# Performance work log

Measured on AMD Instinct MI355X. Metric: run time of the kernel, lower is better.

Reference implementation:

```python
import jax, jax.numpy as jnp
import numpy as np

NUM_GRAPHS = 64


def gcn_conv(x, W, b, src, dst, inv_sqrt_deg, n_nodes):
    # PyG GCNConv: h = D^{-1/2}(A+I)D^{-1/2} X W + b (self-loops already in src/dst)
    h = x @ W  # [N, D_out]
    norm = inv_sqrt_deg[src] * inv_sqrt_deg[dst]  # [E+N]
    msg = h[src] * norm[:, None]  # gather + scale
    agg = jax.ops.segment_sum(msg, dst, num_segments=n_nodes)  # scatter-add
    return agg + b


def setup_inputs() -> dict:
    key = jax.random.key(0)
    ks = jax.random.split(key, 12)
    N, E, D_in, D_h, D_out = 50000, 800000, 256, 256, 128

    def glorot(k, shape):
        lim = np.sqrt(6.0 / (shape[0] + shape[1]))
        return jax.random.uniform(k, shape, jnp.float32, -lim, lim)

    x = jax.random.normal(ks[0], (N, D_in), jnp.float32)
    edge_index = jax.random.randint(ks[1], (2, E), 0, N, jnp.int64)
    batch = jnp.sort(jax.random.randint(ks[2], (N,), 0, NUM_GRAPHS, jnp.int64))
    return {
        "x": x,
        "edge_index": edge_index,
        "batch": batch,
        "W0": glorot(ks[3], (D_in, D_h)), "b0": jnp.zeros((D_h,), jnp.float32),
        "W1": glorot(ks[4], (D_h, D_h)), "b1": jnp.zeros((D_h,), jnp.float32),
        "W2": glorot(ks[5], (D_h, D_h)), "b2": jnp.zeros((D_h,), jnp.float32),
        "fc1_w": glorot(ks[6], (D_h, D_h)), "fc1_b": jnp.zeros((D_h,), jnp.float32),
        "fc2_w": glorot(ks[7], (D_h, D_out)), "fc2_b": jnp.zeros((D_out,), jnp.float32),
    }


def reference(x, edge_index, batch, W0, b0, W1, b1, W2, b2, fc1_w, fc1_b, fc2_w, fc2_b):
    n_nodes = x.shape[0]
    loops = jnp.arange(n_nodes, dtype=edge_index.dtype)
    src = jnp.concatenate([edge_index[0], loops])  # add self-loops
    dst = jnp.concatenate([edge_index[1], loops])
    deg = jax.ops.segment_sum(jnp.ones_like(dst, dtype=x.dtype), dst, num_segments=n_nodes)
    inv_sqrt_deg = jnp.where(deg > 0, jax.lax.rsqrt(jnp.maximum(deg, 1.0)), 0.0)

    h = jax.nn.relu(gcn_conv(x, W0, b0, src, dst, inv_sqrt_deg, n_nodes))
    h = jax.nn.relu(gcn_conv(h, W1, b1, src, dst, inv_sqrt_deg, n_nodes))
    h = jax.nn.relu(gcn_conv(h, W2, b2, src, dst, inv_sqrt_deg, n_nodes))

    # global_mean_pool over batch segment ids
    sums = jax.ops.segment_sum(h, batch, num_segments=NUM_GRAPHS)
    counts = jax.ops.segment_sum(jnp.ones((n_nodes,), h.dtype), batch, num_segments=NUM_GRAPHS)
    pooled = sums / jnp.maximum(counts, 1.0)[:, None]  # [NUM_GRAPHS, D_h]

    out = jax.nn.relu(pooled @ fc1_w + fc1_b)
    out = out @ fc2_w + fc2_b  # [NUM_GRAPHS, D_out]
    return out
```

## Files before the change

kernel.cpp:

```cpp
#include <hip/hip_runtime.h>
#include <stdint.h>

#define D_FEAT 256
#define NGRAPH 64
#define NSPLIT 8
#define BM 64
#define BK 32
#define LDR 40
#define SCAN_CHUNK 1024

using f32x4 = __attribute__((ext_vector_type(4))) float;
using s16x8 = __attribute__((ext_vector_type(8))) short;
using s16x4 = __attribute__((ext_vector_type(4))) short;
using i32x4 = __attribute__((ext_vector_type(4))) int;

__device__ __forceinline__ unsigned short f2bf(float f) {
  union { float f; unsigned u; } v; v.f = f;
  return (unsigned short)((v.u + 0x7FFFu + ((v.u >> 16) & 1u)) >> 16);
}
__device__ __forceinline__ float bf2f(unsigned short h) {
  union { unsigned u; float f; } v; v.u = ((unsigned)h) << 16; return v.f;
}
__device__ __forceinline__ f32x4 bf4_to_f32(s16x4 v) {
  f32x4 r;
  r.x = bf2f((unsigned short)v.x);
  r.y = bf2f((unsigned short)v.y);
  r.z = bf2f((unsigned short)v.z);
  r.w = bf2f((unsigned short)v.w);
  return r;
}

__global__ void hist_k(const int* __restrict__ dst, int* __restrict__ counts, int E) {
  int e = blockIdx.x * blockDim.x + threadIdx.x;
  if (e < E) atomicAdd(&counts[dst[e]], 1);
}

__global__ __launch_bounds__(256) void bsum_k(const int* __restrict__ counts,
                                              int* __restrict__ bsum, int N) {
  int base = blockIdx.x * SCAN_CHUNK;
  int t = threadIdx.x;
  int idx = base + t * 4;
  int s = 0;
  if (idx + 3 < N) {
    i32x4 v = *(const i32x4*)(counts + idx);
    s = v.x + v.y + v.z + v.w;
  } else {
    for (int j = 0; j < 4; ++j) if (idx + j < N) s += counts[idx + j];
  }
  for (int d = 1; d < 64; d <<= 1) s += __shfl_xor(s, d);
  __shared__ int ws[4];
  if ((t & 63) == 0) ws[t >> 6] = s;
  __syncthreads();
  if (t == 0) bsum[blockIdx.x] = ws[0] + ws[1] + ws[2] + ws[3];
}

__global__ __launch_bounds__(1024) void bscan_k(const int* __restrict__ bsum,
                                                int* __restrict__ boff,
                                                int* __restrict__ offN, int nb) {
  __shared__ int part[1024];
  int t = threadIdx.x;
  int v = (t < nb) ? bsum[t] : 0;
  part[t] = v;
  __syncthreads();
  for (int d = 1; d < 1024; d <<= 1) {
    int u = (t >= d) ? part[t - d] : 0;
    __syncthreads();
    part[t] += u;
    __syncthreads();
  }
  if (t < nb) boff[t] = part[t] - v;
  if (t == 1023) offN[0] = part[1023];
}

__global__ __launch_bounds__(256) void fillscan_k(const int* __restrict__ counts,
                                                  const int* __restrict__ boff,
                                                  int* __restrict__ off, int* __restrict__ cur,
                                                  float* __restrict__ isd, int N) {
  int b = blockIdx.x;
  int base = b * SCAN_CHUNK;
  int t = threadIdx.x;
  int idx = base + t * 4;
  int c[4];
  int s = 0;
  for (int j = 0; j < 4; ++j) {
    c[j] = (idx + j < N) ? counts[idx + j] : 0;
    s += c[j];
  }
  int inc = s;
  int lane = t & 63;
  for (int d = 1; d < 64; d <<= 1) {
    int u = __shfl_up(inc, d);
    if (lane >= d) inc += u;
  }
  __shared__ int wtot[4];
  if (lane == 63) wtot[t >> 6] = inc;
  __syncthreads();
  int woff = 0;
  for (int w = 0; w < (t >> 6); ++w) woff += wtot[w];
  int ex = boff[b] + woff + inc - s;
  for (int j = 0; j < 4; ++j) {
    int i = idx + j;
    if (i < N) {
      off[i] = ex;
      cur[i] = ex;
      isd[i] = rsqrtf((float)(c[j] + 1));
      ex += c[j];
    }
  }
}

__global__ void fill_k(const int* __restrict__ src, const int* __restrict__ dst,
                       int* __restrict__ cur, int* __restrict__ csr, int E) {
  int e = blockIdx.x * blockDim.x + threadIdx.x;
  if (e < E) {
    int d = dst[e];
    int pos = atomicAdd(&cur[d], 1);
    csr[pos] = src[e];
  }
}

__global__ void wconv_k(const float* __restrict__ W0, const float* __restrict__ W1,
                        const float* __restrict__ W2, unsigned short* __restrict__ Wt) {
  int idx = blockIdx.x * blockDim.x + threadIdx.x;
  int w = idx >> 16; int r = idx & 65535;
  int k = r >> 8, n = r & 255;
  const float* W = (w == 0) ? W0 : (w == 1) ? W1 : W2;
  Wt[(size_t)w * 65536 + n * 256 + k] = f2bf(W[k * 256 + n]);
}

template <bool F32IN>
__global__ __launch_bounds__(256) void gemm_k(const void* __restrict__ Xv,
                                              const unsigned short* __restrict__ Wt,
                                              unsigned short* __restrict__ P,
                                              const float* __restrict__ isd, int M) {
  __shared__ __align__(16) short As[BM * LDR];
  __shared__ __align__(16) short Bs[D_FEAT * LDR];
  int t = threadIdx.x;
  int lane = t & 63;
  int wave = t >> 6;
  int row0 = blockIdx.x * BM;
  int l15 = lane & 15;
  int l4  = lane >> 4;

  f32x4 acc[4][4];
  for (int m = 0; m < 4; ++m)
    for (int n = 0; n < 4; ++n)
      acc[m][n] = (f32x4){0.f, 0.f, 0.f, 0.f};

  for (int k0 = 0; k0 < D_FEAT; k0 += BK) {
    if constexpr (F32IN) {
      const float* X = (const float*)Xv;
      for (int i = 0; i < 2; ++i) {
        int g = t + i * 256;
        int r = g >> 3, c4 = g & 7;
        int grow = row0 + r;
        f32x4 v = (f32x4){0.f, 0.f, 0.f, 0.f};
        if (grow < M) v = *(const f32x4*)(X + (size_t)grow * D_FEAT + k0 + c4 * 4);
        s16x4 b;
        b.x = (short)f2bf(v.x); b.y = (short)f2bf(v.y);
        b.z = (short)f2bf(v.z); b.w = (short)f2bf(v.w);
        *(s16x4*)&As[r * LDR + c4 * 4] = b;
      }
    } else {
      const unsigned short* X = (const unsigned short*)Xv;
      int r = t >> 2, c = t & 3;
      int grow = row0 + r;
      s16x8 v = {0, 0, 0, 0, 0, 0, 0, 0};
      if (grow < M) v = *(const s16x8*)(X + (size_t)grow * D_FEAT + k0 + c * 8);
      *(s16x8*)&As[r * LDR + c * 8] = v;
    }
    for (int i = 0; i < 4; ++i) {
      int g = t + i * 256;
      int n = g >> 2, c = g & 3;
      i32x4 v = *(const i32x4*)(Wt + (size_t)n * D_FEAT + k0 + c * 8);
      *(i32x4*)&Bs[n * LDR + c * 8] = v;
    }
    __syncthreads();
    s16x8 a[4], b[4];
    for (int m = 0; m < 4; ++m)
      a[m] = *(const s16x8*)&As[(m * 16 + l15) * LDR + l4 * 8];
    for (int n = 0; n < 4; ++n)
      b[n] = *(const s16x8*)&Bs[(wave * 64 + n * 16 + l15) * LDR + l4 * 8];
    for (int m = 0; m < 4; ++m)
      for (int n = 0; n < 4; ++n)
        acc[m][n] = __builtin_amdgcn_mfma_f32_16x16x32_bf16(a[m], b[n], acc[m][n], 0, 0, 0);
    __syncthreads();
  }

  for (int m = 0; m < 4; ++m) {
    int rbase = row0 + m * 16 + l4 * 4;
    for (int r = 0; r < 4; ++r) {
      int row = rbase + r;
      if (row >= M) continue;
      float sc = isd[row];
      for (int n = 0; n < 4; ++n) {
        int col = wave * 64 + n * 16 + l15;
        P[(size_t)row * D_FEAT + col] = f2bf(acc[m][n][r] * sc);
      }
    }
  }
}

__global__ __launch_bounds__(256) void agg_k(const unsigned short* __restrict__ P,
                                             const int* __restrict__ csr,
                                             const int* __restrict__ off,
                                             const float* __restrict__ isd,
                                             const float* __restrict__ bias,
                                             unsigned short* __restrict__ H, int N) {
  int gid = blockIdx.x * blockDim.x + threadIdx.x;
  int node = gid >> 6;
  int lane = gid & 63;
  if (node >= N) return;
  const s16x4* P4 = (const s16x4*)P;
  f32x4 acc = bf4_to_f32(P4[(size_t)node * 64 + lane]);
  int lo = off[node], hi = off[node + 1];
  int e = lo;
  for (; e + 3 < hi; e += 4) {
    int s0 = csr[e], s1 = csr[e + 1], s2 = csr[e + 2], s3 = csr[e + 3];
    s16x4 v0 = P4[(size_t)s0 * 64 + lane];
    s16x4 v1 = P4[(size_t)s1 * 64 + lane];
    s16x4 v2 = P4[(size_t)s2 * 64 + lane];
    s16x4 v3 = P4[(size_t)s3 * 64 + lane];
    acc += bf4_to_f32(v0);
    acc += bf4_to_f32(v1);
    acc += bf4_to_f32(v2);
    acc += bf4_to_f32(v3);
  }
  for (; e < hi; ++e) {
    acc += bf4_to_f32(P4[(size_t)csr[e] * 64 + lane]);
  }
  float sc = isd[node];
  f32x4 bb = *(const f32x4*)(bias + lane * 4);
  s16x4 o;
  o.x = (short)f2bf(fmaxf(acc.x * sc + bb.x, 0.f));
  o.y = (short)f2bf(fmaxf(acc.y * sc + bb.y, 0.f));
  o.z = (short)f2bf(fmaxf(acc.z * sc + bb.z, 0.f));
  o.w = (short)f2bf(fmaxf(acc.w * sc + bb.w, 0.f));
  ((s16x4*)H)[(size_t)node * 64 + lane] = o;
}

__device__ __forceinline__ int lower_bound_batch(const int* __restrict__ b, int N, int v) {
  int lo = 0, hi = N;
  while (lo < hi) { int mid = (lo + hi) >> 1; if (b[mid] < v) lo = mid + 1; else hi = mid; }
  return lo;
}

__global__ __launch_bounds__(256) void pool_k(const unsigned short* __restrict__ H,
                                              const int* __restrict__ batch,
                                              float* __restrict__ pp, int N) {
  int g = blockIdx.x >> 3;
  int s = blockIdx.x & (NSPLIT - 1);
  int c = threadIdx.x;
  int lo = lower_bound_batch(batch, N, g);
  int hi = lower_bound_batch(batch, N, g + 1);
  int len = hi - lo;
  int slo = lo + (int)(((long long)len * s) >> 3);
  int shi = lo + (int)(((long long)len * (s + 1)) >> 3);
  float sum = 0.f;
  for (int i = slo; i < shi; ++i) sum += bf2f(H[(size_t)i * D_FEAT + c]);
  pp[(g * NSPLIT + s) * D_FEAT + c] = sum;
}

__global__ __launch_bounds__(256) void fc_k(const float* __restrict__ pp,
                                            const int* __restrict__ batch,
                                            const float* __restrict__ fc1w, const float* __restrict__ fc1b,
                                            const float* __restrict__ fc2w, const float* __restrict__ fc2b,
                                            float* __restrict__ out, int N) {
  __shared__ float pl[D_FEAT];
  __shared__ float h1[D_FEAT];
  int g = blockIdx.x, j = threadIdx.x;
  int lo = lower_bound_batch(batch, N, g);
  int hi = lower_bound_batch(batch, N, g + 1);
  float cnt = fmaxf((float)(hi - lo), 1.f);
  float sum = 0.f;
  for (int s = 0; s < NSPLIT; ++s) sum += pp[(g * NSPLIT + s) * D_FEAT + j];
  pl[j] = sum / cnt;
  __syncthreads();
  float a = fc1b[j];
  for (int k = 0; k < D_FEAT; ++k) a += pl[k] * fc1w[k * D_FEAT + j];
  h1[j] = fmaxf(a, 0.f);
  __syncthreads();
  if (j < 128) {
    float o = fc2b[j];
    for (int k = 0; k < D_FEAT; ++k) o += h1[k] * fc2w[k * 128 + j];
    out[g * 128 + j] = o;
  }
}

extern "C" void kernel_launch(void* const* d_in, const int* in_sizes, int n_in,
                              void* d_out, int out_size, void* d_ws, size_t ws_size,
                              hipStream_t stream) {
  const float* x    = (const float*)d_in[0];
  const int*   ei   = (const int*)d_in[1];
  const int*   batch= (const int*)d_in[2];
  const float* W0   = (const float*)d_in[3];
  const float* b0   = (const float*)d_in[4];
  const float* W1   = (const float*)d_in[5];
  const float* b1   = (const float*)d_in[6];
  const float* W2   = (const float*)d_in[7];
  const float* b2   = (const float*)d_in[8];
  const float* fc1w = (const float*)d_in[9];
  const float* fc1b = (const float*)d_in[10];
  const float* fc2w = (const float*)d_in[11];
  const float* fc2b = (const float*)d_in[12];
  float* out = (float*)d_out;

  int N = in_sizes[0] / D_FEAT;
  int E = in_sizes[1] / 2;
  const int* srcE = ei;
  const int* dstE = ei + E;
  int nb = (N + SCAN_CHUNK - 1) / SCAN_CHUNK;

  char* w = (char*)d_ws;
  auto alloc = [&](size_t bytes) { char* p = w; w += (bytes + 255) & ~(size_t)255; return p; };
  int*   counts = (int*)  alloc((size_t)N * 4);
  int*   off    = (int*)  alloc((size_t)(N + 1) * 4);
  int*   cur    = (int*)  alloc((size_t)N * 4);
  float* isd    = (float*)alloc((size_t)N * 4);
  int*   csr    = (int*)  alloc((size_t)E * 4);
  int*   bsum   = (int*)  alloc((size_t)nb * 4);
  int*   boff   = (int*)  alloc((size_t)nb * 4);
  unsigned short* Wt = (unsigned short*)alloc((size_t)3 * 65536 * 2);
  unsigned short* P = (unsigned short*)alloc((size_t)N * D_FEAT * 2);
  unsigned short* H = (unsigned short*)alloc((size_t)N * D_FEAT * 2);
  float* pp     = (float*)alloc((size_t)NGRAPH * NSPLIT * D_FEAT * 4);

  hipMemsetAsync(counts, 0, (size_t)N * 4, stream);
  hist_k<<<(E + 255) / 256, 256, 0, stream>>>(dstE, counts, E);
  bsum_k<<<nb, 256, 0, stream>>>(counts, bsum, N);
  bscan_k<<<1, 1024, 0, stream>>>(bsum, boff, off + N, nb);
  fillscan_k<<<nb, 256, 0, stream>>>(counts, boff, off, cur, isd, N);
  fill_k<<<(E + 255) / 256, 256, 0, stream>>>(srcE, dstE, cur, csr, E);
  wconv_k<<<768, 256, 0, stream>>>(W0, W1, W2, Wt);

  int gblocks = (N + BM - 1) / BM;
  int ablocks = (N * 64 + 255) / 256;

  gemm_k<true> <<<gblocks, 256, 0, stream>>>(x, Wt,             P, isd, N);
  agg_k        <<<ablocks, 256, 0, stream>>>(P, csr, off, isd, b0, H, N);
  gemm_k<false><<<gblocks, 256, 0, stream>>>(H, Wt + 65536,     P, isd, N);
  agg_k        <<<ablocks, 256, 0, stream>>>(P, csr, off, isd, b1, H, N);
  gemm_k<false><<<gblocks, 256, 0, stream>>>(H, Wt + 2 * 65536, P, isd, N);
  agg_k        <<<ablocks, 256, 0, stream>>>(P, csr, off, isd, b2, H, N);

  pool_k<<<NGRAPH * NSPLIT, 256, 0, stream>>>(H, batch, pp, N);
  fc_k  <<<NGRAPH, 256, 0, stream>>>(pp, batch, fc1w, fc1b, fc2w, fc2b, out, N);
}
```

Before: 409.1 us.

## Pad CSR rows to even length and aggregate two neighbors per wave with 16B loads

Each node's CSR segment is padded to an even edge count, with padding entries pointing to an extra zero row appended to P and H. The aggregation kernel splits the wave into two halves. Each half gathers a different neighbor with 16-byte vector loads, and the halves are combined with a cross-lane shuffle. This aims to double memory-level parallelism and widen the gather loads. In exchange it adds an init kernel, padded storage, wasted gathers on the pad rows, and a reduction step where half the wave sits idle at write-out.

```diff
diff --git a/kernel.cpp b/kernel.cpp
--- a/kernel.cpp
+++ b/kernel.cpp
@@ -21,14 +21,6 @@
 __device__ __forceinline__ float bf2f(unsigned short h) {
   union { unsigned u; float f; } v; v.u = ((unsigned)h) << 16; return v.f;
 }
-__device__ __forceinline__ f32x4 bf4_to_f32(s16x4 v) {
-  f32x4 r;
-  r.x = bf2f((unsigned short)v.x);
-  r.y = bf2f((unsigned short)v.y);
-  r.z = bf2f((unsigned short)v.z);
-  r.w = bf2f((unsigned short)v.w);
-  return r;
-}
 
 __global__ void hist_k(const int* __restrict__ dst, int* __restrict__ counts, int E) {
   int e = blockIdx.x * blockDim.x + threadIdx.x;
@@ -41,11 +33,8 @@
   int t = threadIdx.x;
   int idx = base + t * 4;
   int s = 0;
-  if (idx + 3 < N) {
-    i32x4 v = *(const i32x4*)(counts + idx);
-    s = v.x + v.y + v.z + v.w;
-  } else {
-    for (int j = 0; j < 4; ++j) if (idx + j < N) s += counts[idx + j];
+  for (int j = 0; j < 4; ++j) {
+    if (idx + j < N) { int c = counts[idx + j]; s += c + (c & 1); }
   }
   for (int d = 1; d < 64; d <<= 1) s += __shfl_xor(s, d);
   __shared__ int ws[4];
@@ -80,11 +69,12 @@
   int base = b * SCAN_CHUNK;
   int t = threadIdx.x;
   int idx = base + t * 4;
-  int c[4];
+  int c[4], cp[4];
   int s = 0;
   for (int j = 0; j < 4; ++j) {
     c[j] = (idx + j < N) ? counts[idx + j] : 0;
-    s += c[j];
+    cp[j] = c[j] + (c[j] & 1);
+    s += cp[j];
   }
   int inc = s;
   int lane = t & 63;
@@ -104,8 +94,23 @@
       off[i] = ex;
       cur[i] = ex;
       isd[i] = rsqrtf((float)(c[j] + 1));
-      ex += c[j];
+      ex += cp[j];
     }
+  }
+}
+
+__global__ __launch_bounds__(256) void csrinit_k(int* __restrict__ csr, int cap4,
+                                                 unsigned int* __restrict__ Prow,
+                                                 unsigned int* __restrict__ Hrow, int N) {
+  int t = blockIdx.x * blockDim.x + threadIdx.x;
+  if (t < cap4) {
+    i32x4 v = (i32x4){N, N, N, N};
+    ((i32x4*)csr)[t] = v;
+  }
+  if (blockIdx.x == 0) {
+    int j = threadIdx.x;
+    if (j < 128) Prow[j] = 0u;
+    else Hrow[j - 128] = 0u;
   }
 }
 
@@ -209,34 +214,58 @@
                                              unsigned short* __restrict__ H, int N) {
   int gid = blockIdx.x * blockDim.x + threadIdx.x;
   int node = gid >> 6;
+  if (node >= N) return;
   int lane = gid & 63;
-  if (node >= N) return;
-  const s16x4* P4 = (const s16x4*)P;
-  f32x4 acc = bf4_to_f32(P4[(size_t)node * 64 + lane]);
+  int half = lane >> 5;
+  int col  = lane & 31;
+  const s16x8* P8 = (const s16x8*)P;
+
+  float acc[8];
+  {
+    int si = half ? N : node;
+    s16x8 v = P8[(size_t)si * 32 + col];
+    for (int j = 0; j < 8; ++j) acc[j] = bf2f((unsigned short)v[j]);
+  }
+
   int lo = off[node], hi = off[node + 1];
   int e = lo;
-  for (; e + 3 < hi; e += 4) {
-    int s0 = csr[e], s1 = csr[e + 1], s2 = csr[e + 2], s3 = csr[e + 3];
-    s16x4 v0 = P4[(size_t)s0 * 64 + lane];
-    s16x4 v1 = P4[(size_t)s1 * 64 + lane];
-    s16x4 v2 = P4[(size_t)s2 * 64 + lane];
-    s16x4 v3 = P4[(size_t)s3 * 64 + lane];
-    acc += bf4_to_f32(v0);
-    acc += bf4_to_f32(v1);
-    acc += bf4_to_f32(v2);
-    acc += bf4_to_f32(v3);
-  }
-  for (; e < hi; ++e) {
-    acc += bf4_to_f32(P4[(size_t)csr[e] * 64 + lane]);
-  }
-  float sc = isd[node];
-  f32x4 bb = *(const f32x4*)(bias + lane * 4);
-  s16x4 o;
-  o.x = (short)f2bf(fmaxf(acc.x * sc + bb.x, 0.f));
-  o.y = (short)f2bf(fmaxf(acc.y * sc + bb.y, 0.f));
-  o.z = (short)f2bf(fmaxf(acc.z * sc + bb.z, 0.f));
-  o.w = (short)f2bf(fmaxf(acc.w * sc + bb.w, 0.f));
-  ((s16x4*)H)[(size_t)node * 64 + lane] = o;
+  for (; e + 8 <= hi; e += 8) {
+    int i0 = csr[e + 0 + half];
+    int i1 = csr[e + 2 + half];
+    int i2 = csr[e + 4 + half];
+    int i3 = csr[e + 6 + half];
+    s16x8 v0 = P8[(size_t)i0 * 32 + col];
+    s16x8 v1 = P8[(size_t)i1 * 32 + col];
+    s16x8 v2 = P8[(size_t)i2 * 32 + col];
+    s16x8 v3 = P8[(size_t)i3 * 32 + col];
+    for (int j = 0; j < 8; ++j) acc[j] += bf2f((unsigned short)v0[j]);
+    for (int j = 0; j < 8; ++j) acc[j] += bf2f((unsigned short)v1[j]);
+    for (int j = 0; j < 8; ++j) acc[j] += bf2f((unsigned short)v2[j]);
+    for (int j = 0; j < 8; ++j) acc[j] += bf2f((unsigned short)v3[j]);
+  }
+  for (; e < hi; e += 2) {
+    int i = csr[e + half];
+    s16x8 v = P8[(size_t)i * 32 + col];
+    for (int j = 0; j < 8; ++j) acc[j] += bf2f((unsigned short)v[j]);
+  }
+
+  for (int j = 0; j < 8; ++j) acc[j] += __shfl_xor(acc[j], 32);
+
+  if (half == 0) {
+    float sc = isd[node];
+    f32x4 b0 = *(const f32x4*)(bias + col * 8);
+    f32x4 b1 = *(const f32x4*)(bias + col * 8 + 4);
+    s16x8 o;
+    o[0] = (short)f2bf(fmaxf(acc[0] * sc + b0.x, 0.f));
+    o[1] = (short)f2bf(fmaxf(acc[1] * sc + b0.y, 0.f));
+    o[2] = (short)f2bf(fmaxf(acc[2] * sc + b0.z, 0.f));
+    o[3] = (short)f2bf(fmaxf(acc[3] * sc + b0.w, 0.f));
+    o[4] = (short)f2bf(fmaxf(acc[4] * sc + b1.x, 0.f));
+    o[5] = (short)f2bf(fmaxf(acc[5] * sc + b1.y, 0.f));
+    o[6] = (short)f2bf(fmaxf(acc[6] * sc + b1.z, 0.f));
+    o[7] = (short)f2bf(fmaxf(acc[7] * sc + b1.w, 0.f));
+    ((s16x8*)H)[(size_t)node * 32 + col] = o;
+  }
 }
 
 __device__ __forceinline__ int lower_bound_batch(const int* __restrict__ b, int N, int v) {
@@ -310,6 +339,7 @@
   const int* srcE = ei;
   const int* dstE = ei + E;
   int nb = (N + SCAN_CHUNK - 1) / SCAN_CHUNK;
+  int Ecap = E + N;
 
   char* w = (char*)d_ws;
   auto alloc = [&](size_t bytes) { char* p = w; w += (bytes + 255) & ~(size_t)255; return p; };
@@ -317,12 +347,12 @@
   int*   off    = (int*)  alloc((size_t)(N + 1) * 4);
   int*   cur    = (int*)  alloc((size_t)N * 4);
   float* isd    = (float*)alloc((size_t)N * 4);
-  int*   csr    = (int*)  alloc((size_t)E * 4);
+  int*   csr    = (int*)  alloc((size_t)(Ecap + 4) * 4);
   int*   bsum   = (int*)  alloc((size_t)nb * 4);
   int*   boff   = (int*)  alloc((size_t)nb * 4);
   unsigned short* Wt = (unsigned short*)alloc((size_t)3 * 65536 * 2);
-  unsigned short* P = (unsigned short*)alloc((size_t)N * D_FEAT * 2);
-  unsigned short* H = (unsigned short*)alloc((size_t)N * D_FEAT * 2);
+  unsigned short* P = (unsigned short*)alloc((size_t)(N + 1) * D_FEAT * 2);
+  unsigned short* H = (unsigned short*)alloc((size_t)(N + 1) * D_FEAT * 2);
   float* pp     = (float*)alloc((size_t)NGRAPH * NSPLIT * D_FEAT * 4);
 
   hipMemsetAsync(counts, 0, (size_t)N * 4, stream);
@@ -330,6 +360,9 @@
   bsum_k<<<nb, 256, 0, stream>>>(counts, bsum, N);
   bscan_k<<<1, 1024, 0, stream>>>(bsum, boff, off + N, nb);
   fillscan_k<<<nb, 256, 0, stream>>>(counts, boff, off, cur, isd, N);
+  int cap4 = (Ecap + 3) / 4;
+  csrinit_k<<<(cap4 + 255) / 256, 256, 0, stream>>>(csr, cap4,
+      (unsigned int*)(P + (size_t)N * D_FEAT), (unsigned int*)(H + (size_t)N * D_FEAT), N);
   fill_k<<<(E + 255) / 256, 256, 0, stream>>>(srcE, dstE, cur, csr, E);
   wconv_k<<<768, 256, 0, stream>>>(W0, W1, W2, Wt);
 
```

After: 408.3 us. Within noise of the previous version (-0.2%).

## Split feature matrices into 32-column slabs and parallelize aggregation across edges

Applied to the files above, without the earlier changes.

P and H move to a slab layout: eight 32-column slabs, each holding N+1 rows, with a zeroed sentinel row at index N. Each GEMM reads and writes this layout. The aggregation kernel now gives one wave to a (node, slab) pair and spreads 16 edges across lane groups, each loading 16 bytes, then reduces with shuffles. The aim is better cache locality for the random gathers, since each slab is 3.2MB, and more memory-level parallelism per node. The cost is 8x more waves, shuffle reductions, and partly idle lanes on nodes with few edges.

```diff
diff --git a/kernel.cpp b/kernel.cpp
--- a/kernel.cpp
+++ b/kernel.cpp
@@ -21,14 +21,6 @@
 __device__ __forceinline__ float bf2f(unsigned short h) {
   union { unsigned u; float f; } v; v.u = ((unsigned)h) << 16; return v.f;
 }
-__device__ __forceinline__ f32x4 bf4_to_f32(s16x4 v) {
-  f32x4 r;
-  r.x = bf2f((unsigned short)v.x);
-  r.y = bf2f((unsigned short)v.y);
-  r.z = bf2f((unsigned short)v.z);
-  r.w = bf2f((unsigned short)v.w);
-  return r;
-}
 
 __global__ void hist_k(const int* __restrict__ dst, int* __restrict__ counts, int E) {
   int e = blockIdx.x * blockDim.x + threadIdx.x;
@@ -41,11 +33,8 @@
   int t = threadIdx.x;
   int idx = base + t * 4;
   int s = 0;
-  if (idx + 3 < N) {
-    i32x4 v = *(const i32x4*)(counts + idx);
-    s = v.x + v.y + v.z + v.w;
-  } else {
-    for (int j = 0; j < 4; ++j) if (idx + j < N) s += counts[idx + j];
+  for (int j = 0; j < 4; ++j) {
+    if (idx + j < N) s += counts[idx + j];
   }
   for (int d = 1; d < 64; d <<= 1) s += __shfl_xor(s, d);
   __shared__ int ws[4];
@@ -109,6 +98,19 @@
   }
 }
 
+__global__ void zrow_k(unsigned int* __restrict__ Pu, unsigned int* __restrict__ Hu,
+                       int NP1, int N) {
+  int j = threadIdx.x;
+  if (j < 128) {
+    int s = j >> 4, u = j & 15;
+    Pu[((size_t)s * NP1 + N) * 16 + u] = 0u;
+  } else {
+    int j2 = j - 128;
+    int s = j2 >> 4, u = j2 & 15;
+    Hu[((size_t)s * NP1 + N) * 16 + u] = 0u;
+  }
+}
+
 __global__ void fill_k(const int* __restrict__ src, const int* __restrict__ dst,
                        int* __restrict__ cur, int* __restrict__ csr, int E) {
   int e = blockIdx.x * blockDim.x + threadIdx.x;
@@ -132,7 +134,7 @@
 __global__ __launch_bounds__(256) void gemm_k(const void* __restrict__ Xv,
                                               const unsigned short* __restrict__ Wt,
                                               unsigned short* __restrict__ P,
-                                              const float* __restrict__ isd, int M) {
+                                              const float* __restrict__ isd, int M, int NP1) {
   __shared__ __align__(16) short As[BM * LDR];
   __shared__ __align__(16) short Bs[D_FEAT * LDR];
   int t = threadIdx.x;
@@ -166,7 +168,7 @@
       int r = t >> 2, c = t & 3;
       int grow = row0 + r;
       s16x8 v = {0, 0, 0, 0, 0, 0, 0, 0};
-      if (grow < M) v = *(const s16x8*)(X + (size_t)grow * D_FEAT + k0 + c * 8);
+      if (grow < M) v = *(const s16x8*)(X + ((size_t)(k0 >> 5) * NP1 + grow) * 32 + c * 8);
       *(s16x8*)&As[r * LDR + c * 8] = v;
     }
     for (int i = 0; i < 4; ++i) {
@@ -195,7 +197,7 @@
       float sc = isd[row];
       for (int n = 0; n < 4; ++n) {
         int col = wave * 64 + n * 16 + l15;
-        P[(size_t)row * D_FEAT + col] = f2bf(acc[m][n][r] * sc);
+        P[((size_t)(col >> 5) * NP1 + row) * 32 + (col & 31)] = f2bf(acc[m][n][r] * sc);
       }
     }
   }
@@ -206,37 +208,54 @@
                                              const int* __restrict__ off,
                                              const float* __restrict__ isd,
                                              const float* __restrict__ bias,
-                                             unsigned short* __restrict__ H, int N) {
-  int gid = blockIdx.x * blockDim.x + threadIdx.x;
-  int node = gid >> 6;
-  int lane = gid & 63;
+                                             unsigned short* __restrict__ H,
+                                             int N, int NP1) {
+  int s = blockIdx.x & 7;
+  int node = (blockIdx.x >> 3) * 4 + (threadIdx.x >> 6);
   if (node >= N) return;
-  const s16x4* P4 = (const s16x4*)P;
-  f32x4 acc = bf4_to_f32(P4[(size_t)node * 64 + lane]);
+  int lane = threadIdx.x & 63;
+  int g = lane >> 2;
+  int c = lane & 3;
+  const s16x8* Pb = (const s16x8*)P + (size_t)s * NP1 * 4;
+
+  float acc[8];
+  {
+    int si = (g == 0) ? node : N;
+    s16x8 v = Pb[(size_t)si * 4 + c];
+    for (int j = 0; j < 8; ++j) acc[j] = bf2f((unsigned short)v[j]);
+  }
+
   int lo = off[node], hi = off[node + 1];
-  int e = lo;
-  for (; e + 3 < hi; e += 4) {
-    int s0 = csr[e], s1 = csr[e + 1], s2 = csr[e + 2], s3 = csr[e + 3];
-    s16x4 v0 = P4[(size_t)s0 * 64 + lane];
-    s16x4 v1 = P4[(size_t)s1 * 64 + lane];
-    s16x4 v2 = P4[(size_t)s2 * 64 + lane];
-    s16x4 v3 = P4[(size_t)s3 * 64 + lane];
-    acc += bf4_to_f32(v0);
-    acc += bf4_to_f32(v1);
-    acc += bf4_to_f32(v2);
-    acc += bf4_to_f32(v3);
-  }
-  for (; e < hi; ++e) {
-    acc += bf4_to_f32(P4[(size_t)csr[e] * 64 + lane]);
-  }
-  float sc = isd[node];
-  f32x4 bb = *(const f32x4*)(bias + lane * 4);
-  s16x4 o;
-  o.x = (short)f2bf(fmaxf(acc.x * sc + bb.x, 0.f));
-  o.y = (short)f2bf(fmaxf(acc.y * sc + bb.y, 0.f));
-  o.z = (short)f2bf(fmaxf(acc.z * sc + bb.z, 0.f));
-  o.w = (short)f2bf(fmaxf(acc.w * sc + bb.w, 0.f));
-  ((s16x4*)H)[(size_t)node * 64 + lane] = o;
+  for (int e = lo; e < hi; e += 16) {
+    int ee = e + g;
+    int idx = (ee < hi) ? __builtin_nontemporal_load(csr + ee) : N;
+    s16x8 v = Pb[(size_t)idx * 4 + c];
+    for (int j = 0; j < 8; ++j) acc[j] += bf2f((unsigned short)v[j]);
+  }
+
+  for (int j = 0; j < 8; ++j) {
+    acc[j] += __shfl_xor(acc[j], 4);
+    acc[j] += __shfl_xor(acc[j], 8);
+    acc[j] += __shfl_xor(acc[j], 16);
+    acc[j] += __shfl_xor(acc[j], 32);
+  }
+
+  if (lane < 4) {
+    float sc = isd[node];
+    const float* bp = bias + s * 32 + c * 8;
+    f32x4 b0 = *(const f32x4*)bp;
+    f32x4 b1 = *(const f32x4*)(bp + 4);
+    s16x8 o;
+    o[0] = (short)f2bf(fmaxf(acc[0] * sc + b0.x, 0.f));
+    o[1] = (short)f2bf(fmaxf(acc[1] * sc + b0.y, 0.f));
+    o[2] = (short)f2bf(fmaxf(acc[2] * sc + b0.z, 0.f));
+    o[3] = (short)f2bf(fmaxf(acc[3] * sc + b0.w, 0.f));
+    o[4] = (short)f2bf(fmaxf(acc[4] * sc + b1.x, 0.f));
+    o[5] = (short)f2bf(fmaxf(acc[5] * sc + b1.y, 0.f));
+    o[6] = (short)f2bf(fmaxf(acc[6] * sc + b1.z, 0.f));
+    o[7] = (short)f2bf(fmaxf(acc[7] * sc + b1.w, 0.f));
+    ((s16x8*)H)[((size_t)s * NP1 + node) * 4 + c] = o;
+  }
 }
 
 __device__ __forceinline__ int lower_bound_batch(const int* __restrict__ b, int N, int v) {
@@ -247,18 +266,19 @@
 
 __global__ __launch_bounds__(256) void pool_k(const unsigned short* __restrict__ H,
                                               const int* __restrict__ batch,
-                                              float* __restrict__ pp, int N) {
+                                              float* __restrict__ pp, int N, int NP1) {
   int g = blockIdx.x >> 3;
   int s = blockIdx.x & (NSPLIT - 1);
-  int c = threadIdx.x;
+  int cf = threadIdx.x;
+  const unsigned short* Hs = H + (size_t)(cf >> 5) * NP1 * 32 + (cf & 31);
   int lo = lower_bound_batch(batch, N, g);
   int hi = lower_bound_batch(batch, N, g + 1);
   int len = hi - lo;
   int slo = lo + (int)(((long long)len * s) >> 3);
   int shi = lo + (int)(((long long)len * (s + 1)) >> 3);
   float sum = 0.f;
-  for (int i = slo; i < shi; ++i) sum += bf2f(H[(size_t)i * D_FEAT + c]);
-  pp[(g * NSPLIT + s) * D_FEAT + c] = sum;
+  for (int i = slo; i < shi; ++i) sum += bf2f(Hs[(size_t)i * 32]);
+  pp[(g * NSPLIT + s) * D_FEAT + cf] = sum;
 }
 
 __global__ __launch_bounds__(256) void fc_k(const float* __restrict__ pp,
@@ -310,6 +330,7 @@
   const int* srcE = ei;
   const int* dstE = ei + E;
   int nb = (N + SCAN_CHUNK - 1) / SCAN_CHUNK;
+  int NP1 = N + 1;
 
   char* w = (char*)d_ws;
   auto alloc = [&](size_t bytes) { char* p = w; w += (bytes + 255) & ~(size_t)255; return p; };
@@ -321,8 +342,8 @@
   int*   bsum   = (int*)  alloc((size_t)nb * 4);
   int*   boff   = (int*)  alloc((size_t)nb * 4);
   unsigned short* Wt = (unsigned short*)alloc((size_t)3 * 65536 * 2);
-  unsigned short* P = (unsigned short*)alloc((size_t)N * D_FEAT * 2);
-  unsigned short* H = (unsigned short*)alloc((size_t)N * D_FEAT * 2);
+  unsigned short* P = (unsigned short*)alloc((size_t)NP1 * D_FEAT * 2);
+  unsigned short* H = (unsigned short*)alloc((size_t)NP1 * D_FEAT * 2);
   float* pp     = (float*)alloc((size_t)NGRAPH * NSPLIT * D_FEAT * 4);
 
   hipMemsetAsync(counts, 0, (size_t)N * 4, stream);
@@ -330,19 +351,20 @@
   bsum_k<<<nb, 256, 0, stream>>>(counts, bsum, N);
   bscan_k<<<1, 1024, 0, stream>>>(bsum, boff, off + N, nb);
   fillscan_k<<<nb, 256, 0, stream>>>(counts, boff, off, cur, isd, N);
+  zrow_k<<<1, 256, 0, stream>>>((unsigned int*)P, (unsigned int*)H, NP1, N);
   fill_k<<<(E + 255) / 256, 256, 0, stream>>>(srcE, dstE, cur, csr, E);
   wconv_k<<<768, 256, 0, stream>>>(W0, W1, W2, Wt);
 
   int gblocks = (N + BM - 1) / BM;
-  int ablocks = (N * 64 + 255) / 256;
-
-  gemm_k<true> <<<gblocks, 256, 0, stream>>>(x, Wt,             P, isd, N);
-  agg_k        <<<ablocks, 256, 0, stream>>>(P, csr, off, isd, b0, H, N);
-  gemm_k<false><<<gblocks, 256, 0, stream>>>(H, Wt + 65536,     P, isd, N);
-  agg_k        <<<ablocks, 256, 0, stream>>>(P, csr, off, isd, b1, H, N);
-  gemm_k<false><<<gblocks, 256, 0, stream>>>(H, Wt + 2 * 65536, P, isd, N);
-  agg_k        <<<ablocks, 256, 0, stream>>>(P, csr, off, isd, b2, H, N);
-
-  pool_k<<<NGRAPH * NSPLIT, 256, 0, stream>>>(H, batch, pp, N);
+  int ablocks = 8 * ((N + 3) / 4);
+
+  gemm_k<true> <<<gblocks, 256, 0, stream>>>(x, Wt,             P, isd, N, NP1);
+  agg_k        <<<ablocks, 256, 0, stream>>>(P, csr, off, isd, b0, H, N, NP1);
+  gemm_k<false><<<gblocks, 256, 0, stream>>>(H, Wt + 65536,     P, isd, N, NP1);
+  agg_k        <<<ablocks, 256, 0, stream>>>(P, csr, off, isd, b1, H, N, NP1);
+  gemm_k<false><<<gblocks, 256, 0, stream>>>(H, Wt + 2 * 65536, P, isd, N, NP1);
+  agg_k        <<<ablocks, 256, 0, stream>>>(P, csr, off, isd, b2, H, N, NP1);
+
+  pool_k<<<NGRAPH * NSPLIT, 256, 0, stream>>>(H, batch, pp, N, NP1);
   fc_k  <<<NGRAPH, 256, 0, stream>>>(pp, batch, fc1w, fc1b, fc2w, fc2b, out, N);
 }
```

Result: slower. 703.5 us (+72.0%).
